# Optimization experiments

Measured on AMD Instinct MI355X. Metric: run time of the kernel, lower is better.

Reference implementation:

```python
import jax, jax.numpy as jnp
import numpy as np

B, T, E = 4, 2048, 256
H = 8
HD = E // H
FE = 4
L = 4
EPS = 1e-5


def _layernorm(x, g, b):
    mu = jnp.mean(x, axis=-1, keepdims=True)
    var = jnp.mean((x - mu) ** 2, axis=-1, keepdims=True)
    return (x - mu) * jax.lax.rsqrt(var + EPS) * g + b


def setup_inputs() -> dict:
    key = jax.random.key(0)
    ks = jax.random.split(key, 14)
    s = 0.02
    inp = {
        "x": jax.random.normal(ks[0], (B, T, E), dtype=jnp.float32),
        "qkv_w": jax.random.normal(ks[1], (L, E, 3 * E), dtype=jnp.float32) * s,
        "qkv_b": jnp.zeros((L, 3 * E), jnp.float32),
        "out_w": jax.random.normal(ks[2], (L, E, E), dtype=jnp.float32) * s,
        "out_b": jnp.zeros((L, E), jnp.float32),
        "ff1_w": jax.random.normal(ks[3], (L, E, FE * E), dtype=jnp.float32) * s,
        "ff1_b": jnp.zeros((L, FE * E), jnp.float32),
        "ff2_w": jax.random.normal(ks[4], (L, FE * E, E), dtype=jnp.float32) * s,
        "ff2_b": jnp.zeros((L, E), jnp.float32),
        "ln1_g": jnp.ones((L, E), jnp.float32),
        "ln1_b": jnp.zeros((L, E), jnp.float32),
        "ln2_g": jnp.ones((L, E), jnp.float32),
        "ln2_b": jnp.zeros((L, E), jnp.float32),
    }
    return inp


def _fourier_pe(x):
    # freqs over even indices: 10000^(-i/E), i = 0,2,...,E-2  -> E/2 freqs
    freqs = jnp.power(10000.0, -jnp.arange(0, E, 2, dtype=jnp.float32) / E)
    pos = jnp.arange(T, dtype=jnp.float32)[:, None]          # (T,1)
    sinusoid = pos * freqs[None, :]                            # (T, E/2)
    pe = jnp.concatenate([jnp.sin(sinusoid), jnp.cos(sinusoid)], axis=-1)  # (T,E)
    return x + pe[None, :, :]


def _forward(x, qkv_w, qkv_b, out_w, out_b, ff1_w, ff1_b, ff2_w, ff2_b,
             ln1_g, ln1_b, ln2_g, ln2_b):
    x = _fourier_pe(x)
    scale = 1.0 / np.sqrt(HD)
    for i in range(L):
        # attention (dropout = identity at eval)
        qkv = x @ qkv_w[i] + qkv_b[i]                          # (B,T,3E)
        qkv = qkv.reshape(B, T, H, 3, HD)                      # chunk of 3*hd -> (3,hd)
        q, k, v = qkv[..., 0, :], qkv[..., 1, :], qkv[..., 2, :]  # (B,T,H,HD)
        scores = jnp.einsum("bqhd,bkhd->bhqk", q, k) * scale   # (B,H,T,T)
        w = jax.nn.softmax(scores, axis=-1)
        attn = jnp.einsum("bhqk,bkhd->bqhd", w, v).reshape(B, T, E)
        attn = attn @ out_w[i] + out_b[i]
        x = _layernorm(x + attn, ln1_g[i], ln1_b[i])
        # feedforward
        h = jax.nn.relu(x @ ff1_w[i] + ff1_b[i])
        ff = h @ ff2_w[i] + ff2_b[i]
        x = _layernorm(x + ff, ln2_g[i], ln2_b[i])
    return x


def reference(x, qkv_w, qkv_b, out_w, out_b, ff1_w, ff1_b, ff2_w, ff2_b,
              ln1_g, ln1_b, ln2_g, ln2_b):
    return _forward(x, qkv_w, qkv_b, out_w, out_b, ff1_w, ff1_b, ff2_w, ff2_b,
                    ln1_g, ln1_b, ln2_g, ln2_b)
```

## Files before the change

### kernel.cpp

```cpp
#include <hip/hip_runtime.h>
#include <hip/hip_bf16.h>
#include <stdint.h>

typedef unsigned short u16;
typedef _Float16 f16;
typedef short vs8 __attribute__((ext_vector_type(8)));
typedef float vf4 __attribute__((ext_vector_type(4)));
typedef _Float16 vh2 __attribute__((ext_vector_type(2)));
typedef _Float16 vh4 __attribute__((ext_vector_type(4)));
typedef _Float16 vh8 __attribute__((ext_vector_type(8)));
typedef __fp16 hw2 __attribute__((ext_vector_type(2)));


__device__ __forceinline__ void gload16(const u16* g, u16* l) {
  __builtin_amdgcn_global_load_lds((const __attribute__((address_space(1))) void*)g,
                                   (__attribute__((address_space(3))) void*)l,
                                   16, 0, 0);
}

__device__ __forceinline__ float fexp2(float x) {
#if __has_builtin(__builtin_amdgcn_exp2f)
  return __builtin_amdgcn_exp2f(x);
#else
  return __expf(x * 0.69314718056f);
#endif
}

__global__ void pe_kernel(const float* __restrict__ x, __hip_bfloat16* __restrict__ Xb) {
  int gid = blockIdx.x * 256 + threadIdx.x;
  int row = gid >> 6;
  int e0 = (gid & 63) * 4;
  int t = row & 2047;
  int f0 = (e0 < 128) ? e0 : (e0 - 128);
  const float c = -13.287712379549449f / 128.0f;
  const float inv2pi = 0.15915494309189535f;
  float4 xv = *(const float4*)(x + (size_t)row * 256 + e0);
  u16 o[4];
#pragma unroll
  for (int j = 0; j < 4; ++j) {
    float freq = fexp2(c * (float)(f0 + j));
    float rev = (float)t * freq * inv2pi;
    rev = rev - floorf(rev);
    float pe = (e0 < 128) ? __builtin_amdgcn_sinf(rev) : __builtin_amdgcn_cosf(rev);
    float xin = (j == 0) ? xv.x : (j == 1) ? xv.y : (j == 2) ? xv.z : xv.w;
    __hip_bfloat16 hb = __float2bfloat16(xin + pe);
    o[j] = *(u16*)&hb;
  }
  *(uint2*)((u16*)Xb + (size_t)row * 256 + e0) = *(uint2*)o;
}

__global__ void transpose_cast_all(
    const float* __restrict__ w0, const float* __restrict__ w1,
    const float* __restrict__ w2, const float* __restrict__ w3,
    u16* __restrict__ o0, u16* __restrict__ o1,
    u16* __restrict__ o2, u16* __restrict__ o3) {
  __shared__ float tile[32][33];
  int flat = blockIdx.x;
  int layer = flat / 768;
  int r = flat - layer * 768;
  const float* ip; u16* op; int K, N, kt, nt;
  if (r < 192)      {              ip = w0; op = o0; K = 256;  N = 768;  kt = r & 7;  nt = r >> 3; }
  else if (r < 256) { int q=r-192; ip = w1; op = o1; K = 256;  N = 256;  kt = q & 7;  nt = q >> 3; }
  else if (r < 512) { int q=r-256; ip = w2; op = o2; K = 256;  N = 1024; kt = q & 7;  nt = q >> 3; }
  else              { int q=r-512; ip = w3; op = o3; K = 1024; N = 256;  kt = q & 31; nt = q >> 5; }
  ip += (size_t)layer * K * N;
  op += (size_t)layer * N * K;
  int k0 = kt * 32, n0 = nt * 32;
  int tx = threadIdx.x, ty = threadIdx.y;
#pragma unroll
  for (int rr = 0; rr < 4; ++rr) {
    int k = ty + rr * 8;
    tile[k][tx] = ip[(size_t)(k0 + k) * N + (n0 + tx)];
  }
  __syncthreads();
#pragma unroll
  for (int rr = 0; rr < 4; ++rr) {
    int n = ty + rr * 8;
    __hip_bfloat16 v = __float2bfloat16(tile[tx][n]);
    op[(size_t)(n0 + n) * K + (k0 + tx)] = *(u16*)&v;
  }
}

__global__ __launch_bounds__(256, 2) void gemm_relu(
    const u16* __restrict__ A, const u16* __restrict__ Bt,
    const float* __restrict__ bias, __hip_bfloat16* __restrict__ outB,
    int M, int N, int K) {
  __shared__ u16 As[128 * 64];
  __shared__ u16 Bs[128 * 64];
  int tid = threadIdx.x;
  int wave = tid >> 6, lane = tid & 63;
  int wm = wave & 1, wn = wave >> 1;
  int m0 = blockIdx.y * 128, n0 = blockIdx.x * 128;
  int lr = lane & 15, lq = lane >> 4;

  vf4 acc[4][4];
#pragma unroll
  for (int i = 0; i < 4; ++i)
#pragma unroll
    for (int j = 0; j < 4; ++j) {
      acc[i][j][0] = 0.f; acc[i][j][1] = 0.f; acc[i][j][2] = 0.f; acc[i][j][3] = 0.f;
    }

  int srow = tid >> 3;
  int scol = (tid & 7) * 8;
  const u16* ag = A + (size_t)(m0 + srow) * K + scol;
  const u16* bg = Bt + (size_t)(n0 + srow) * K + scol;
  u16* al = As + srow * 64 + scol;
  u16* bl = Bs + srow * 64 + scol;
  const size_t rstride32 = (size_t)32 * K;

  for (int k0 = 0; k0 < K; k0 += 64) {
#pragma unroll
    for (int r = 0; r < 4; ++r) {
      gload16(ag + k0 + r * rstride32, al + r * 32 * 64);
      gload16(bg + k0 + r * rstride32, bl + r * 32 * 64);
    }
    __syncthreads();
#pragma unroll
    for (int kk = 0; kk < 2; ++kk) {
      vs8 av[4], bv[4];
#pragma unroll
      for (int i = 0; i < 4; ++i)
        av[i] = *(const vs8*)&As[(wm * 64 + i * 16 + lr) * 64 + kk * 32 + lq * 8];
#pragma unroll
      for (int j = 0; j < 4; ++j)
        bv[j] = *(const vs8*)&Bs[(wn * 64 + j * 16 + lr) * 64 + kk * 32 + lq * 8];
#pragma unroll
      for (int i = 0; i < 4; ++i)
#pragma unroll
        for (int j = 0; j < 4; ++j)
          acc[i][j] = __builtin_amdgcn_mfma_f32_16x16x32_bf16(av[i], bv[j], acc[i][j], 0, 0, 0);
    }
    __syncthreads();
  }

#pragma unroll
  for (int i = 0; i < 4; ++i) {
    int row0 = m0 + wm * 64 + i * 16 + lq * 4;
#pragma unroll
    for (int j = 0; j < 4; ++j) {
      int col = n0 + wn * 64 + j * 16 + lr;
      float bb = bias[col];
#pragma unroll
      for (int r = 0; r < 4; ++r) {
        size_t idx = (size_t)(row0 + r) * N + col;
        outB[idx] = __float2bfloat16(fmaxf(acc[i][j][r] + bb, 0.0f));
      }
    }
  }
}

__global__ __launch_bounds__(256, 2) void gemm_qkv128(
    const u16* __restrict__ A, const u16* __restrict__ Bt,
    const float* __restrict__ bias, f16* __restrict__ outH,
    int M, int N, int K) {
  __shared__ u16 As[128 * 64];
  __shared__ u16 Bs[128 * 64];
  int tid = threadIdx.x;
  int wave = tid >> 6, lane = tid & 63;
  int wm = wave & 1, wn = wave >> 1;
  int m0 = blockIdx.y * 128, n0 = blockIdx.x * 128;
  int lr = lane & 15, lq = lane >> 4;

  vf4 acc[4][4];
#pragma unroll
  for (int i = 0; i < 4; ++i)
#pragma unroll
    for (int j = 0; j < 4; ++j) {
      acc[i][j][0] = 0.f; acc[i][j][1] = 0.f; acc[i][j][2] = 0.f; acc[i][j][3] = 0.f;
    }

  int srow = tid >> 3;
  int scol = (tid & 7) * 8;
  const u16* ag = A + (size_t)(m0 + srow) * K + scol;
  const u16* bg = Bt + (size_t)(n0 + srow) * K + scol;
  u16* al = As + srow * 64 + scol;
  u16* bl = Bs + srow * 64 + scol;
  const size_t rstride32 = (size_t)32 * K;

  for (int k0 = 0; k0 < K; k0 += 64) {
#pragma unroll
    for (int r = 0; r < 4; ++r) {
      gload16(ag + k0 + r * rstride32, al + r * 32 * 64);
      gload16(bg + k0 + r * rstride32, bl + r * 32 * 64);
    }
    __syncthreads();
#pragma unroll
    for (int kk = 0; kk < 2; ++kk) {
      vs8 av[4], bv[4];
#pragma unroll
      for (int i = 0; i < 4; ++i)
        av[i] = *(const vs8*)&As[(wm * 64 + i * 16 + lr) * 64 + kk * 32 + lq * 8];
#pragma unroll
      for (int j = 0; j < 4; ++j)
        bv[j] = *(const vs8*)&Bs[(wn * 64 + j * 16 + lr) * 64 + kk * 32 + lq * 8];
#pragma unroll
      for (int i = 0; i < 4; ++i)
#pragma unroll
        for (int j = 0; j < 4; ++j)
          acc[i][j] = __builtin_amdgcn_mfma_f32_16x16x32_bf16(av[i], bv[j], acc[i][j], 0, 0, 0);
    }
    __syncthreads();
  }

#pragma unroll
  for (int i = 0; i < 4; ++i) {
    int row0 = m0 + wm * 64 + i * 16 + lq * 4;
#pragma unroll
    for (int j = 0; j < 4; ++j) {
      int col = n0 + wn * 64 + j * 16 + lr;
      float bb = bias[col];
#pragma unroll
      for (int r = 0; r < 4; ++r)
        outH[(size_t)(row0 + r) * N + col] = (f16)(acc[i][j][r] + bb);
    }
  }
}

__global__ __launch_bounds__(512, 2) void gemm_ln(
    const u16* __restrict__ A, const u16* __restrict__ Bt,
    const float* __restrict__ bias, const __hip_bfloat16* __restrict__ res,
    const float* __restrict__ gam, const float* __restrict__ bet,
    __hip_bfloat16* __restrict__ outB, float* __restrict__ outF, int K,
    const f16* __restrict__ OfA, const float* __restrict__ lf) {
  __shared__ u16 As[32 * 64];
  __shared__ u16 Bs[256 * 64];
  __shared__ float ps[4][32], ps2[4][32], mur[32], rsr[32];
  __shared__ float invs[8][32];
  int tid = threadIdx.x;
  int wave = tid >> 6, lane = tid & 63;
  int wm = wave & 1, wn = wave >> 1;
  int lr = lane & 15, lq = lane >> 4;
  int m0 = blockIdx.x * 32;

  vf4 acc[4];
#pragma unroll
  for (int j = 0; j < 4; ++j) { acc[j][0]=0.f; acc[j][1]=0.f; acc[j][2]=0.f; acc[j][3]=0.f; }

  int sr = tid >> 3, sc = (tid & 7) * 8;
  const u16* ag = A + (size_t)(m0 + sr) * K + sc;
  const u16* bg = Bt + (size_t)sr * K + sc;
  u16* al = As + sr * 64 + sc;
  u16* bl = Bs + sr * 64 + sc;

  if (OfA) {
    if (tid < 256) {
      int h = tid >> 5, rl = tid & 31;
      int row = m0 + rl, bb_ = row >> 11, t = row & 2047;
      int g = bb_ * 8 + h;
      invs[h][rl] = 1.0f / (lf[g * 2048 + t] + lf[65536 + g * 2048 + t]);
    }
    __syncthreads();
  }

  for (int k0 = 0; k0 < K; k0 += 64) {
    if (tid < 256) {
      if (OfA) {
        size_t off = (size_t)(m0 + sr) * 256 + k0 + sc;
        vh8 a0 = *(const vh8*)(OfA + off);
        vh8 a1 = *(const vh8*)(OfA + 2097152 + off);
        float inv = invs[(k0 + sc) >> 5][sr];
        union { vs8 v; u16 u[8]; } pk;
#pragma unroll
        for (int j = 0; j < 8; ++j) {
          __hip_bfloat16 hb = __float2bfloat16(((float)a0[j] + (float)a1[j]) * inv);
          pk.u[j] = *(u16*)&hb;
        }
        *(vs8*)al = pk.v;
      } else {
        gload16(ag + k0, al);
      }
    }
#pragma unroll
    for (int r = 0; r < 4; ++r)
      gload16(bg + k0 + (size_t)(r * 64) * K, bl + r * 64 * 64);
    __syncthreads();
#pragma unroll
    for (int kk = 0; kk < 2; ++kk) {
      vs8 av, bv[4];
      av = *(const vs8*)&As[(wm * 16 + lr) * 64 + kk * 32 + lq * 8];
#pragma unroll
      for (int j = 0; j < 4; ++j)
        bv[j] = *(const vs8*)&Bs[(wn * 64 + j * 16 + lr) * 64 + kk * 32 + lq * 8];
#pragma unroll
      for (int j = 0; j < 4; ++j)
        acc[j] = __builtin_amdgcn_mfma_f32_16x16x32_bf16(av, bv[j], acc[j], 0, 0, 0);
    }
    __syncthreads();
  }

  float sum_[4], sq_[4];
#pragma unroll
  for (int r = 0; r < 4; ++r) { sum_[r] = 0.f; sq_[r] = 0.f; }
#pragma unroll
  for (int j = 0; j < 4; ++j) {
    int col = wn * 64 + j * 16 + lr;
    float bb = bias[col];
#pragma unroll
    for (int r = 0; r < 4; ++r) {
      int row = m0 + wm * 16 + lq * 4 + r;
      float v = acc[j][r] + bb + __bfloat162float(res[(size_t)row * 256 + col]);
      acc[j][r] = v;
      sum_[r] += v;
      sq_[r] += v * v;
    }
  }
#pragma unroll
  for (int r = 0; r < 4; ++r) {
#pragma unroll
    for (int m = 1; m <= 8; m <<= 1) {
      sum_[r] += __shfl_xor(sum_[r], m);
      sq_[r]  += __shfl_xor(sq_[r], m);
    }
  }
  if (lr == 0) {
#pragma unroll
    for (int r = 0; r < 4; ++r) {
      int rl = wm * 16 + lq * 4 + r;
      ps[wn][rl] = sum_[r];
      ps2[wn][rl] = sq_[r];
    }
  }
  __syncthreads();
  if (tid < 32) {
    float s = ps[0][tid] + ps[1][tid] + ps[2][tid] + ps[3][tid];
    float s2 = ps2[0][tid] + ps2[1][tid] + ps2[2][tid] + ps2[3][tid];
    float mu = s * (1.0f / 256.0f);
    float var = s2 * (1.0f / 256.0f) - mu * mu;
    mur[tid] = mu;
    rsr[tid] = rsqrtf(var + 1e-5f);
  }
  __syncthreads();
#pragma unroll
  for (int r = 0; r < 4; ++r) {
    int rl = wm * 16 + lq * 4 + r;
    float mu = mur[rl], rs = rsr[rl];
    int row = m0 + rl;
#pragma unroll
    for (int j = 0; j < 4; ++j) {
      int col = wn * 64 + j * 16 + lr;
      float o = (acc[j][r] - mu) * rs * gam[col] + bet[col];
      size_t idx = (size_t)row * 256 + col;
      outB[idx] = __float2bfloat16(o);
      if (outF) outF[idx] = o;
    }
  }
}

__global__ __launch_bounds__(512, 4) void attn_mfma(const f16* __restrict__ qkv,
                                                    f16* __restrict__ Of,
                                                    float* __restrict__ lf) {
  __shared__ __align__(16) u16 lds[2][9344];
  int tid = threadIdx.x;
  int wave = tid >> 6, lane = tid & 63;
  int lr = lane & 15, quad = lane >> 4;

  int id = blockIdx.x;
  int xcd = id & 7, slot = id >> 3;
  int grp = xcd * 4 + (slot & 3);
  int qt = (slot >> 2) & 7;
  int split = slot >> 5;
  int b = grp >> 3, h = grp & 7;
  int q0 = qt * 256;
  int kv0 = split << 10;
  int rowbase = b * 2048;
  const f16* base_bh = qkv + (size_t)rowbase * 768 + h * 96;

  vh8 qf[2];
#pragma unroll
  for (int nt = 0; nt < 2; ++nt) {
    int qr = q0 + wave * 32 + nt * 16 + lr;
    vh8 t = *(const vh8*)(base_bh + (size_t)qr * 768 + quad * 8);
#pragma unroll
    for (int j = 0; j < 8; ++j) t[j] = t[j] * (f16)0.25508682f;
    qf[nt] = t;
  }

  vf4 O[2][2], lO[2];
#pragma unroll
  for (int a = 0; a < 2; ++a) {
    lO[a][0]=0.f; lO[a][1]=0.f; lO[a][2]=0.f; lO[a][3]=0.f;
#pragma unroll
    for (int d = 0; d < 2; ++d) { O[a][d][0]=0.f; O[a][d][1]=0.f; O[a][d][2]=0.f; O[a][d][3]=0.f; }
  }

  int srK = tid >> 2;
  int scK = (tid & 3) * 8;
  const f16* kg = base_bh + (size_t)(kv0 + srK) * 768 + 32 + scK;
  int kvp = tid >> 3;
  int d4 = (tid & 7) * 4;
  const f16* vg = base_bh + (size_t)(kv0 + kvp * 2) * 768 + 64 + d4;

  const vf4 z4 = {0.f, 0.f, 0.f, 0.f};
  const vh4 onesh = {(f16)1.0f, (f16)1.0f, (f16)1.0f, (f16)1.0f};
  const size_t cstep = (size_t)128 * 768;

  {
    vh8 k0 = *(const vh8*)kg;
    *(vh8*)&lds[0][srK * 40 + scK] = k0;
    vh4 a = *(const vh4*)vg;
    vh4 bb = *(const vh4*)(vg + 768);
    f16* vt0 = (f16*)&lds[0][5120];
#pragma unroll
    for (int i = 0; i < 4; ++i) {
      vh2 pr; pr[0] = a[i]; pr[1] = bb[i];
      *(vh2*)(vt0 + (d4 + i) * 132 + kvp * 2) = pr;
    }
  }
  __syncthreads();

  for (int c = 0; c < 8; ++c) {
    int cur = c & 1;
    const f16* Ks = (const f16*)&lds[cur][0];
    const f16* VT = (const f16*)&lds[cur][5120];

    vh8 kn; vh4 va, vb;
    if (c < 7) {
      kn = *(const vh8*)(kg + (size_t)(c + 1) * cstep);
      const f16* vp = vg + (size_t)(c + 1) * cstep;
      va = *(const vh4*)vp;
      vb = *(const vh4*)(vp + 768);
    }

#pragma unroll
    for (int t16 = 0; t16 < 8; ++t16) {
      vh8 ak = *(const vh8*)&Ks[(t16 * 16 + lr) * 40 + quad * 8];
      vf4 s0 = __builtin_amdgcn_mfma_f32_16x16x32_f16(ak, qf[0], z4, 0, 0, 0);
      vf4 s1 = __builtin_amdgcn_mfma_f32_16x16x32_f16(ak, qf[1], z4, 0, 0, 0);
      vh4 p0, p1;
      ((hw2*)&p0)[0] = __builtin_amdgcn_cvt_pkrtz(fexp2(s0[0]), fexp2(s0[1]));
      ((hw2*)&p0)[1] = __builtin_amdgcn_cvt_pkrtz(fexp2(s0[2]), fexp2(s0[3]));
      ((hw2*)&p1)[0] = __builtin_amdgcn_cvt_pkrtz(fexp2(s1[0]), fexp2(s1[1]));
      ((hw2*)&p1)[1] = __builtin_amdgcn_cvt_pkrtz(fexp2(s1[2]), fexp2(s1[3]));
      vh4 vf0 = *(const vh4*)&VT[(0 * 16 + lr) * 132 + t16 * 16 + quad * 4];
      vh4 vf1 = *(const vh4*)&VT[(1 * 16 + lr) * 132 + t16 * 16 + quad * 4];
      O[0][0] = __builtin_amdgcn_mfma_f32_16x16x16f16(p0, vf0, O[0][0], 0, 0, 0);
      O[0][1] = __builtin_amdgcn_mfma_f32_16x16x16f16(p0, vf1, O[0][1], 0, 0, 0);
      O[1][0] = __builtin_amdgcn_mfma_f32_16x16x16f16(p1, vf0, O[1][0], 0, 0, 0);
      O[1][1] = __builtin_amdgcn_mfma_f32_16x16x16f16(p1, vf1, O[1][1], 0, 0, 0);
      lO[0] = __builtin_amdgcn_mfma_f32_16x16x16f16(p0, onesh, lO[0], 0, 0, 0);
      lO[1] = __builtin_amdgcn_mfma_f32_16x16x16f16(p1, onesh, lO[1], 0, 0, 0);
    }

    if (c < 7) {
      *(vh8*)&lds[cur ^ 1][srK * 40 + scK] = kn;
      f16* vt1 = (f16*)&lds[cur ^ 1][5120];
#pragma unroll
      for (int i = 0; i < 4; ++i) {
        vh2 pr; pr[0] = va[i]; pr[1] = vb[i];
        *(vh2*)(vt1 + (d4 + i) * 132 + kvp * 2) = pr;
      }
    }
    __syncthreads();
  }

#pragma unroll
  for (int nt = 0; nt < 2; ++nt) {
#pragma unroll
    for (int r = 0; r < 4; ++r) {
      int tq = q0 + wave * 32 + nt * 16 + quad * 4 + r;
      if (lr == 0) lf[split * 65536 + grp * 2048 + tq] = lO[nt][r];
      int row = rowbase + tq;
#pragma unroll
      for (int dt = 0; dt < 2; ++dt) {
        int col = h * 32 + dt * 16 + lr;
        Of[(size_t)split * 2097152 + (size_t)row * 256 + col] = (f16)O[nt][dt][r];
      }
    }
  }
}

extern "C" void kernel_launch(void* const* d_in, const int* in_sizes, int n_in,
                              void* d_out, int out_size, void* d_ws, size_t ws_size,
                              hipStream_t stream) {
  (void)in_sizes; (void)n_in; (void)out_size; (void)ws_size;
  const float* x     = (const float*)d_in[0];
  const float* qkv_b = (const float*)d_in[2];
  const float* out_b = (const float*)d_in[4];
  const float* ff1_b = (const float*)d_in[6];
  const float* ff2_b = (const float*)d_in[8];
  const float* ln1_g = (const float*)d_in[9];
  const float* ln1_b = (const float*)d_in[10];
  const float* ln2_g = (const float*)d_in[11];
  const float* ln2_b = (const float*)d_in[12];

  char* ws = (char*)d_ws;
  f16*            Of    = (f16*)(ws + 0);
  __hip_bfloat16* Xb    = (__hip_bfloat16*)(ws + 8388608);
  float*          lf    = (float*)(ws + 12582912);
  f16*            qkvH  = (f16*)(ws + 25165824);
  __hip_bfloat16* hB    = (__hip_bfloat16*)(ws + 20971520);
  u16* qkvwT = (u16*)(ws + 37748736);
  u16* outwT = (u16*)(ws + 39321600);
  u16* ff1wT = (u16*)(ws + 39845888);
  u16* ff2wT = (u16*)(ws + 41943040);

  pe_kernel<<<2048, 256, 0, stream>>>(x, Xb);
  transpose_cast_all<<<3072, dim3(32, 8), 0, stream>>>(
      (const float*)d_in[1], (const float*)d_in[3], (const float*)d_in[5], (const float*)d_in[7],
      qkvwT, outwT, ff1wT, ff2wT);

  for (int l = 0; l < 4; ++l) {
    gemm_qkv128<<<dim3(6, 64), 256, 0, stream>>>((const u16*)Xb, qkvwT + (size_t)l * 768 * 256,
        qkv_b + l * 768, qkvH, 8192, 768, 256);
    attn_mfma<<<512, 512, 0, stream>>>(qkvH, Of, lf);
    gemm_ln<<<256, 512, 0, stream>>>(nullptr, outwT + (size_t)l * 256 * 256,
        out_b + l * 256, Xb, ln1_g + l * 256, ln1_b + l * 256, Xb, nullptr, 256, Of, lf);
    gemm_relu<<<dim3(8, 64), 256, 0, stream>>>((const u16*)Xb, ff1wT + (size_t)l * 1024 * 256,
        ff1_b + l * 1024, hB, 8192, 1024, 256);
    float* lnout = (l == 3) ? (float*)d_out : nullptr;
    gemm_ln<<<256, 512, 0, stream>>>((const u16*)hB, ff2wT + (size_t)l * 256 * 1024,
        ff2_b + l * 256, Xb, ln2_g + l * 256, ln2_b + l * 256, Xb, lnout, 1024, nullptr, nullptr);
  }
}
```

Before: 440.8 us.

## Swizzle LDS GEMM tiles, shrink QKV tile to 64 rows, raise attention MFMA priority

Applies an XOR swizzle to the global-to-LDS column mapping in all GEMM kernels so MFMA operand reads from LDS avoid bank conflicts. The swizzle is applied on the global source address because global_load_lds writes LDS linearly. Shrinks the QKV GEMM M-tile from 128 to 64 rows, doubling the grid and raising occupancy to 3 blocks per SIMD. Also raises wave priority around the attention MFMA loop with s_setprio. The smaller QKV tile gives up some data reuse per block.

```diff
diff --git a/kernel.cpp b/kernel.cpp
--- a/kernel.cpp
+++ b/kernel.cpp
@@ -10,6 +10,7 @@
 typedef _Float16 vh4 __attribute__((ext_vector_type(4)));
 typedef _Float16 vh8 __attribute__((ext_vector_type(8)));
 typedef __fp16 hw2 __attribute__((ext_vector_type(2)));
+
 
 
 __device__ __forceinline__ void gload16(const u16* g, u16* l) {
@@ -92,6 +93,7 @@
   int wm = wave & 1, wn = wave >> 1;
   int m0 = blockIdx.y * 128, n0 = blockIdx.x * 128;
   int lr = lane & 15, lq = lane >> 4;
+  int swz = (lr & 7) << 3;
 
   vf4 acc[4][4];
 #pragma unroll
@@ -102,11 +104,12 @@
     }
 
   int srow = tid >> 3;
-  int scol = (tid & 7) * 8;
-  const u16* ag = A + (size_t)(m0 + srow) * K + scol;
-  const u16* bg = Bt + (size_t)(n0 + srow) * K + scol;
-  u16* al = As + srow * 64 + scol;
-  u16* bl = Bs + srow * 64 + scol;
+  int sc = (tid & 7) * 8;
+  int cswz = (((tid & 7) ^ (srow & 7)) * 8);
+  const u16* ag = A + (size_t)(m0 + srow) * K + cswz;
+  const u16* bg = Bt + (size_t)(n0 + srow) * K + cswz;
+  u16* al = As + srow * 64 + sc;
+  u16* bl = Bs + srow * 64 + sc;
   const size_t rstride32 = (size_t)32 * K;
 
   for (int k0 = 0; k0 < K; k0 += 64) {
@@ -121,10 +124,10 @@
       vs8 av[4], bv[4];
 #pragma unroll
       for (int i = 0; i < 4; ++i)
-        av[i] = *(const vs8*)&As[(wm * 64 + i * 16 + lr) * 64 + kk * 32 + lq * 8];
+        av[i] = *(const vs8*)&As[(wm * 64 + i * 16 + lr) * 64 + ((kk * 32 + lq * 8) ^ swz)];
 #pragma unroll
       for (int j = 0; j < 4; ++j)
-        bv[j] = *(const vs8*)&Bs[(wn * 64 + j * 16 + lr) * 64 + kk * 32 + lq * 8];
+        bv[j] = *(const vs8*)&Bs[(wn * 64 + j * 16 + lr) * 64 + ((kk * 32 + lq * 8) ^ swz)];
 #pragma unroll
       for (int i = 0; i < 4; ++i)
 #pragma unroll
@@ -150,52 +153,53 @@
   }
 }
 
-__global__ __launch_bounds__(256, 2) void gemm_qkv128(
+__global__ __launch_bounds__(256, 3) void gemm_qkv64(
     const u16* __restrict__ A, const u16* __restrict__ Bt,
     const float* __restrict__ bias, f16* __restrict__ outH,
     int M, int N, int K) {
-  __shared__ u16 As[128 * 64];
+  __shared__ u16 As[64 * 64];
   __shared__ u16 Bs[128 * 64];
   int tid = threadIdx.x;
   int wave = tid >> 6, lane = tid & 63;
   int wm = wave & 1, wn = wave >> 1;
-  int m0 = blockIdx.y * 128, n0 = blockIdx.x * 128;
+  int m0 = blockIdx.y * 64, n0 = blockIdx.x * 128;
   int lr = lane & 15, lq = lane >> 4;
-
-  vf4 acc[4][4];
-#pragma unroll
-  for (int i = 0; i < 4; ++i)
-#pragma unroll
-    for (int j = 0; j < 4; ++j) {
-      acc[i][j][0] = 0.f; acc[i][j][1] = 0.f; acc[i][j][2] = 0.f; acc[i][j][3] = 0.f;
-    }
+  int swz = (lr & 7) << 3;
+
+  vf4 acc[2][4];
+#pragma unroll
+  for (int i = 0; i < 2; ++i)
+#pragma unroll
+    for (int j = 0; j < 4; ++j) { acc[i][j][0]=0.f; acc[i][j][1]=0.f; acc[i][j][2]=0.f; acc[i][j][3]=0.f; }
 
   int srow = tid >> 3;
-  int scol = (tid & 7) * 8;
-  const u16* ag = A + (size_t)(m0 + srow) * K + scol;
-  const u16* bg = Bt + (size_t)(n0 + srow) * K + scol;
-  u16* al = As + srow * 64 + scol;
-  u16* bl = Bs + srow * 64 + scol;
+  int sc = (tid & 7) * 8;
+  int cswz = (((tid & 7) ^ (srow & 7)) * 8);
+  const u16* ag = A + (size_t)(m0 + srow) * K + cswz;
+  const u16* bg = Bt + (size_t)(n0 + srow) * K + cswz;
+  u16* al = As + srow * 64 + sc;
+  u16* bl = Bs + srow * 64 + sc;
   const size_t rstride32 = (size_t)32 * K;
 
   for (int k0 = 0; k0 < K; k0 += 64) {
 #pragma unroll
-    for (int r = 0; r < 4; ++r) {
+    for (int r = 0; r < 2; ++r)
       gload16(ag + k0 + r * rstride32, al + r * 32 * 64);
+#pragma unroll
+    for (int r = 0; r < 4; ++r)
       gload16(bg + k0 + r * rstride32, bl + r * 32 * 64);
-    }
     __syncthreads();
 #pragma unroll
     for (int kk = 0; kk < 2; ++kk) {
-      vs8 av[4], bv[4];
-#pragma unroll
-      for (int i = 0; i < 4; ++i)
-        av[i] = *(const vs8*)&As[(wm * 64 + i * 16 + lr) * 64 + kk * 32 + lq * 8];
+      vs8 av[2], bv[4];
+#pragma unroll
+      for (int i = 0; i < 2; ++i)
+        av[i] = *(const vs8*)&As[(wm * 32 + i * 16 + lr) * 64 + ((kk * 32 + lq * 8) ^ swz)];
 #pragma unroll
       for (int j = 0; j < 4; ++j)
-        bv[j] = *(const vs8*)&Bs[(wn * 64 + j * 16 + lr) * 64 + kk * 32 + lq * 8];
-#pragma unroll
-      for (int i = 0; i < 4; ++i)
+        bv[j] = *(const vs8*)&Bs[(wn * 64 + j * 16 + lr) * 64 + ((kk * 32 + lq * 8) ^ swz)];
+#pragma unroll
+      for (int i = 0; i < 2; ++i)
 #pragma unroll
         for (int j = 0; j < 4; ++j)
           acc[i][j] = __builtin_amdgcn_mfma_f32_16x16x32_bf16(av[i], bv[j], acc[i][j], 0, 0, 0);
@@ -204,8 +208,8 @@
   }
 
 #pragma unroll
-  for (int i = 0; i < 4; ++i) {
-    int row0 = m0 + wm * 64 + i * 16 + lq * 4;
+  for (int i = 0; i < 2; ++i) {
+    int row0 = m0 + wm * 32 + i * 16 + lq * 4;
 #pragma unroll
     for (int j = 0; j < 4; ++j) {
       int col = n0 + wn * 64 + j * 16 + lr;
@@ -232,14 +236,17 @@
   int wm = wave & 1, wn = wave >> 1;
   int lr = lane & 15, lq = lane >> 4;
   int m0 = blockIdx.x * 32;
+  int swz = (lr & 7) << 3;
 
   vf4 acc[4];
 #pragma unroll
   for (int j = 0; j < 4; ++j) { acc[j][0]=0.f; acc[j][1]=0.f; acc[j][2]=0.f; acc[j][3]=0.f; }
 
-  int sr = tid >> 3, sc = (tid & 7) * 8;
-  const u16* ag = A + (size_t)(m0 + sr) * K + sc;
-  const u16* bg = Bt + (size_t)sr * K + sc;
+  int sr = tid >> 3;
+  int sc = (tid & 7) * 8;
+  int cswz = (((tid & 7) ^ (sr & 7)) * 8);
+  const u16* ag = A + (size_t)(m0 + sr) * K + cswz;
+  const u16* bg = Bt + (size_t)sr * K + cswz;
   u16* al = As + sr * 64 + sc;
   u16* bl = Bs + sr * 64 + sc;
 
@@ -256,10 +263,10 @@
   for (int k0 = 0; k0 < K; k0 += 64) {
     if (tid < 256) {
       if (OfA) {
-        size_t off = (size_t)(m0 + sr) * 256 + k0 + sc;
+        size_t off = (size_t)(m0 + sr) * 256 + k0 + cswz;
         vh8 a0 = *(const vh8*)(OfA + off);
         vh8 a1 = *(const vh8*)(OfA + 2097152 + off);
-        float inv = invs[(k0 + sc) >> 5][sr];
+        float inv = invs[(k0 + cswz) >> 5][sr];
         union { vs8 v; u16 u[8]; } pk;
 #pragma unroll
         for (int j = 0; j < 8; ++j) {
@@ -278,10 +285,10 @@
 #pragma unroll
     for (int kk = 0; kk < 2; ++kk) {
       vs8 av, bv[4];
-      av = *(const vs8*)&As[(wm * 16 + lr) * 64 + kk * 32 + lq * 8];
+      av = *(const vs8*)&As[(wm * 16 + lr) * 64 + ((kk * 32 + lq * 8) ^ swz)];
 #pragma unroll
       for (int j = 0; j < 4; ++j)
-        bv[j] = *(const vs8*)&Bs[(wn * 64 + j * 16 + lr) * 64 + kk * 32 + lq * 8];
+        bv[j] = *(const vs8*)&Bs[(wn * 64 + j * 16 + lr) * 64 + ((kk * 32 + lq * 8) ^ swz)];
 #pragma unroll
       for (int j = 0; j < 4; ++j)
         acc[j] = __builtin_amdgcn_mfma_f32_16x16x32_bf16(av, bv[j], acc[j], 0, 0, 0);
@@ -422,6 +429,7 @@
       vb = *(const vh4*)(vp + 768);
     }
 
+    __builtin_amdgcn_s_setprio(1);
 #pragma unroll
     for (int t16 = 0; t16 < 8; ++t16) {
       vh8 ak = *(const vh8*)&Ks[(t16 * 16 + lr) * 40 + quad * 8];
@@ -441,6 +449,7 @@
       lO[0] = __builtin_amdgcn_mfma_f32_16x16x16f16(p0, onesh, lO[0], 0, 0, 0);
       lO[1] = __builtin_amdgcn_mfma_f32_16x16x16f16(p1, onesh, lO[1], 0, 0, 0);
     }
+    __builtin_amdgcn_s_setprio(0);
 
     if (c < 7) {
       *(vh8*)&lds[cur ^ 1][srK * 40 + scK] = kn;
@@ -501,7 +510,7 @@
       qkvwT, outwT, ff1wT, ff2wT);
 
   for (int l = 0; l < 4; ++l) {
-    gemm_qkv128<<<dim3(6, 64), 256, 0, stream>>>((const u16*)Xb, qkvwT + (size_t)l * 768 * 256,
+    gemm_qkv64<<<dim3(6, 128), 256, 0, stream>>>((const u16*)Xb, qkvwT + (size_t)l * 768 * 256,
         qkv_b + l * 768, qkvH, 8192, 768, 256);
     attn_mfma<<<512, 512, 0, stream>>>(qkvH, Of, lf);
     gemm_ln<<<256, 512, 0, stream>>>(nullptr, outwT + (size_t)l * 256 * 256,
```

Result: faster. 401.9 us (-8.8%).
